# Kernel optimization log

Measured on AMD Instinct MI355X. Metric: run time of the kernel, lower is better.

## Reference

```python
import jax, jax.numpy as jnp
import numpy as np

B, CDD, HIS, S, L, F, K = 32, 5, 100, 20, 3, 150, 18
NNEWS, RDIM = 10000, 256


def _maxpool3(x):
    # kernel [3,3,3], stride [3,3,3], no padding (torch MaxPool3d default)
    return jax.lax.reduce_window(x, -jnp.inf, jax.lax.max,
                                 (1, 1, 3, 3, 3), (1, 1, 3, 3, 3), 'VALID')


def setup_inputs() -> dict:
    key = jax.random.key(0)
    ks = jax.random.split(key, 10)
    return {
        'cdd_id': jax.random.randint(ks[0], (B, CDD), 0, NNEWS),
        'his_id': jax.random.randint(ks[1], (B, HIS), 0, NNEWS),
        'news_repr_table': jax.random.normal(ks[2], (NNEWS, RDIM), jnp.float32),
        'news_embedding_table': jax.random.normal(ks[3], (NNEWS, S * L * F), jnp.float32),
        'conv1_w': jax.random.normal(ks[4], (32, 3, 3, 3, 3), jnp.float32) * 0.1,
        'conv1_b': jax.random.normal(ks[5], (32,), jnp.float32) * 0.1,
        'conv2_w': jax.random.normal(ks[6], (16, 32, 3, 3, 3), jnp.float32) * 0.1,
        'conv2_b': jax.random.normal(ks[7], (16,), jnp.float32) * 0.1,
        'ltr_w': jax.random.normal(ks[8], (1, 128), jnp.float32) * 0.1,
        'ltr_b': jax.random.normal(ks[9], (1,), jnp.float32) * 0.1,
    }


def reference(cdd_id, his_id, news_repr_table, news_embedding_table,
              conv1_w, conv1_b, conv2_w, conv2_b, ltr_w, ltr_b):
    cdd_repr = news_repr_table[cdd_id]                    # [B,CDD,R]
    his_repr = news_repr_table[his_id]                    # [B,HIS,R]
    cdd_emb = news_embedding_table[cdd_id].reshape(B, CDD, S, L, F)
    his_emb = news_embedding_table[his_id]                # [B,HIS,S*L*F]

    # attention scores; original applies softmax then sorts the (detached)
    # weights -- softmax is monotone per row so argsort on logits is identical
    attn = jnp.einsum('bcr,bhr->bch', cdd_repr, his_repr)  # [B,CDD,HIS]
    topk_idx = jnp.argsort(-attn, axis=-1)[..., :K]        # [B,CDD,K]

    # direct gather (replaces the one_hot @ embedding matmul, same math)
    his_act = his_emb[jnp.arange(B)[:, None, None], topk_idx]  # [B,CDD,K,S*L*F]
    his_act = his_act.reshape(B, CDD, K, S, L, F)

    # fusion tensor at each dilation level
    cdd_t = cdd_emb.transpose(0, 1, 3, 2, 4)       # [B,CDD,L,S,F]
    his_t = his_act.transpose(0, 1, 2, 4, 3, 5)    # [B,CDD,K,L,S,F]
    fusion = jnp.einsum('bclsf,bckltf->bcklst', cdd_t, his_t) / np.sqrt(F).astype(np.float32)
    x = fusion.reshape(B * CDD, K, L, S, S).transpose(0, 2, 1, 3, 4)  # [B*CDD,L,K,S,S]

    dn = ('NCDHW', 'OIDHW', 'NCDHW')
    pad1 = [(1, 1)] * 3
    x = jax.lax.conv_general_dilated(x, conv1_w, (1, 1, 1), pad1, dimension_numbers=dn)
    x = jax.nn.relu(x + conv1_b[None, :, None, None, None])
    x = _maxpool3(x)                                # [B*CDD,32,6,6,6]
    x = jax.lax.conv_general_dilated(x, conv2_w, (1, 1, 1), pad1, dimension_numbers=dn)
    x = jax.nn.relu(x + conv2_b[None, :, None, None, None])
    x = _maxpool3(x)                                # [B*CDD,16,2,2,2]

    feat = x.reshape(B, CDD, -1)                    # [B,CDD,128]
    score = jnp.einsum('bcd,od->bco', feat, ltr_w)[..., 0] + ltr_b[0]  # [B,CDD]
    return jax.nn.log_softmax(score, axis=1)
```

## Files before the change

### kernel.cpp

```cpp
#include <hip/hip_runtime.h>
#include <hip/hip_bf16.h>
#include <math.h>

#define B_    32
#define CDD_  5
#define HIS_  100
#define S_    20
#define L_    3
#define F_    150
#define K_    18
#define RDIM_ 256
#define ROWE_ 9000
#define NBC_  160

typedef __attribute__((ext_vector_type(8))) short short8;
typedef __attribute__((ext_vector_type(4))) float f32x4;

static __device__ __forceinline__ unsigned short f2bf(float x) {
  union { float f; unsigned u; } v; v.f = x;
  unsigned r = v.u + 0x7fffu + ((v.u >> 16) & 1u);
  return (unsigned short)(r >> 16);
}

__global__ __launch_bounds__(256) void attn_topk_kernel(
    const int* __restrict__ cdd_id, const int* __restrict__ his_id,
    const float* __restrict__ repr, int* __restrict__ gid,
    float* __restrict__ score,
    const float* __restrict__ w1, const float* __restrict__ w2,
    float* __restrict__ w1t, float* __restrict__ w2t) {
  int bc = blockIdx.x;
  int b  = bc / CDD_;
  int tid = threadIdx.x, lane = tid & 63, wave = tid >> 6;

  int gidx = bc * 256 + tid;
  if (gidx < 2592) {
    int oc = gidx / 81, j = gidx % 81;
    w1t[j * 32 + oc] = w1[gidx];
  } else if (gidx < 2592 + 13824) {
    int i2 = gidx - 2592;
    int oc = i2 / 864, r = i2 % 864;
    w2t[r * 16 + oc] = w2[i2];
  }

  __shared__ float cddv[RDIM_];
  __shared__ float sattn[128];
  int cid = cdd_id[bc];
  cddv[tid] = repr[(size_t)cid * RDIM_ + tid];
  if (tid < 28) sattn[100 + tid] = -INFINITY;
  __syncthreads();

  float4 cv = *(const float4*)(cddv + lane * 4);
  for (int h = wave; h < HIS_; h += 4) {
    const float4* row = (const float4*)(repr + (size_t)his_id[b * HIS_ + h] * RDIM_);
    float4 rv = row[lane];
    float p = cv.x * rv.x;
    p = fmaf(cv.y, rv.y, p);
    p = fmaf(cv.z, rv.z, p);
    p = fmaf(cv.w, rv.w, p);
    #pragma unroll
    for (int off = 32; off >= 1; off >>= 1) p += __shfl_xor(p, off);
    if (lane == 0) sattn[h] = p;
  }
  __syncthreads();

  if (wave == 0) {
    float v0 = sattn[lane], v1 = sattn[lane + 64];
    for (int k = 0; k < K_; k++) {
      float bv; int bi;
      if (v1 > v0) { bv = v1; bi = lane + 64; } else { bv = v0; bi = lane; }
      #pragma unroll
      for (int off = 32; off >= 1; off >>= 1) {
        float ov = __shfl_xor(bv, off);
        int   oi = __shfl_xor(bi, off);
        if (ov > bv || (ov == bv && oi < bi)) { bv = ov; bi = oi; }
      }
      if (lane == 0) gid[bc * K_ + k] = his_id[b * HIS_ + bi];
      if (bi == lane)      v0 = -INFINITY;
      if (bi == lane + 64) v1 = -INFINITY;
    }
  }
  if (tid == 0) score[bc] = 0.f;
}

__global__ __launch_bounds__(256) void fusion_kernel(
    const int* __restrict__ cdd_id, const int* __restrict__ gid,
    const float* __restrict__ emb, float* __restrict__ x1) {
  int bck = (blockIdx.x & 7) * 360 + (blockIdx.x >> 3);
  int bc = bck / K_, k = bck % K_;
  __shared__ unsigned short a_sh[3 * 32 * 160];
  __shared__ unsigned short b_sh[3 * 32 * 160];
  int tid = threadIdx.x;

  unsigned* az = (unsigned*)a_sh;
  unsigned* bz = (unsigned*)b_sh;
  for (int i = tid; i < 480; i += 256) {
    int l = i / 160, r = i % 160;
    int srow = r / 5, j = r % 5;
    int idx = (l * 32 + srow) * 80 + 75 + j;
    az[idx] = 0u; bz[idx] = 0u;
  }

  const float* crow = emb + (size_t)cdd_id[bc] * ROWE_;
  const float* hrow = emb + (size_t)gid[bck] * ROWE_;
  for (int p = tid; p < 2250; p += 256) {
    int e0 = p * 4;
    int s0 = e0 / 450, r0 = e0 % 450;
    int l0 = r0 / 150, f0 = r0 % 150;
    int e2 = e0 + 2;
    int s2 = e2 / 450, r2 = e2 % 450;
    int l2 = r2 / 150, f2 = r2 % 150;
    float4 cv = *(const float4*)(crow + e0);
    float4 hv = *(const float4*)(hrow + e0);
    int d0 = (l0 * 32 + s0) * 80 + (f0 >> 1);
    int d2 = (l2 * 32 + s2) * 80 + (f2 >> 1);
    az[d0] = (unsigned)f2bf(cv.x) | ((unsigned)f2bf(cv.y) << 16);
    az[d2] = (unsigned)f2bf(cv.z) | ((unsigned)f2bf(cv.w) << 16);
    bz[d0] = (unsigned)f2bf(hv.x) | ((unsigned)f2bf(hv.y) << 16);
    bz[d2] = (unsigned)f2bf(hv.z) | ((unsigned)f2bf(hv.w) << 16);
  }
  __syncthreads();

  int wave = tid >> 6, lane = tid & 63;
  int m15 = lane & 15, quad = lane >> 4;
  const float scale = 0.0816496580927726f;
  for (int j = wave; j < 12; j += 4) {
    int l = j >> 2, mt = (j >> 1) & 1, nt = j & 1;
    f32x4 acc = {0.f, 0.f, 0.f, 0.f};
    int abase = (l * 32 + mt * 16 + m15) * 160 + quad * 8;
    int bbase = (l * 32 + nt * 16 + m15) * 160 + quad * 8;
    #pragma unroll
    for (int kb = 0; kb < 5; kb++) {
      short8 af = *(const short8*)(a_sh + abase + kb * 32);
      short8 bf = *(const short8*)(b_sh + bbase + kb * 32);
      acc = __builtin_amdgcn_mfma_f32_16x16x32_bf16(af, bf, acc, 0, 0, 0);
    }
    int t = nt * 16 + m15;
    if (t < 20) {
      size_t base = ((size_t)(bc * 3 + l) * K_ + k) * 400;
      #pragma unroll
      for (int reg = 0; reg < 4; reg++) {
        int s = mt * 16 + quad * 4 + reg;
        if (s < 20) x1[base + s * 20 + t] = acc[reg] * scale;
      }
    }
  }
}

__global__ __launch_bounds__(256) void conv1_kernel(
    const float* __restrict__ x1, const float* __restrict__ w1t,
    const float* __restrict__ b1, float* __restrict__ p1) {
  int bid = blockIdx.x;
  int n = bid / 6, dp = bid % 6;
  __shared__ float tile[3 * 5 * 22 * 22];
  __shared__ unsigned pooled[32 * 36];
  int tid = threadIdx.x;

  for (int i = tid; i < 7260; i += 256) {
    int c = i / 2420; int r = i % 2420;
    int dd = r / 484; r %= 484;
    int hh = r / 22, ww = r % 22;
    int d = dp * 3 + dd - 1, h = hh - 1, w = ww - 1;
    float v = 0.f;
    if (d >= 0 && d < 18 && h >= 0 && h < 20 && w >= 0 && w < 20)
      v = x1[((size_t)(n * 3 + c) * K_ + d) * 400 + h * 20 + w];
    tile[i] = v;
  }
  for (int i = tid; i < 1152; i += 256) pooled[i] = 0u;
  __syncthreads();

  for (int pos = tid; pos < 972; pos += 256) {
    int dl = pos / 324; int r = pos % 324;
    int h = r / 18, w = r % 18;
    float acc[32];
    #pragma unroll
    for (int oc = 0; oc < 32; oc++) acc[oc] = b1[oc];

    for (int c = 0; c < 3; c++) {
      const float* tc = tile + (c * 5 + dl) * 484 + h * 22 + w;
      const float* wc = w1t + c * 27 * 32;
      #pragma unroll
      for (int kd = 0; kd < 3; kd++)
        #pragma unroll
        for (int kh = 0; kh < 3; kh++)
          #pragma unroll
          for (int kw = 0; kw < 3; kw++) {
            float iv = tc[kd * 484 + kh * 22 + kw];
            const float* wp = wc + (kd * 9 + kh * 3 + kw) * 32;
            #pragma unroll
            for (int oc = 0; oc < 32; oc++) acc[oc] = fmaf(iv, wp[oc], acc[oc]);
          }
    }
    int pbase = (h / 3) * 6 + (w / 3);
    #pragma unroll
    for (int oc = 0; oc < 32; oc++)
      atomicMax(&pooled[oc * 36 + pbase], __float_as_uint(fmaxf(acc[oc], 0.f)));
  }
  __syncthreads();
  for (int i = tid; i < 1152; i += 256) {
    int oc = i / 36; int r = i % 36;
    p1[(size_t)(n * 32 + oc) * 216 + dp * 36 + r] = __uint_as_float(pooled[i]);
  }
}

__global__ __launch_bounds__(256) void conv2_kernel(
    const float* __restrict__ p1, const float* __restrict__ w2t,
    const float* __restrict__ b2, const float* __restrict__ lw,
    float* __restrict__ score) {
  int bid = blockIdx.x;
  int n = bid / 2, og = bid % 2;
  __shared__ float tile[32 * 8 * 8 * 8];
  __shared__ unsigned pooled[64];
  int tid = threadIdx.x;

  for (int i = tid; i < 32 * 512; i += 256) tile[i] = 0.f;
  if (tid < 64) pooled[tid] = 0u;
  __syncthreads();
  for (int i = tid; i < 32 * 216; i += 256) {
    int c = i / 216; int r = i % 216;
    int d = r / 36; r %= 36;
    int h = r / 6, w = r % 6;
    tile[c * 512 + (d + 1) * 64 + (h + 1) * 8 + (w + 1)] =
        p1[(size_t)n * 32 * 216 + i];
  }
  __syncthreads();

  if (tid < 216) {
    int d = tid / 36; int r = tid % 36;
    int h = r / 6, w = r % 6;
    float acc[8];
    #pragma unroll
    for (int oc = 0; oc < 8; oc++) acc[oc] = b2[og * 8 + oc];
    for (int c = 0; c < 32; c++) {
      const float* tc = tile + c * 512 + d * 64 + h * 8 + w;
      const float* wc = w2t + c * 27 * 16 + og * 8;
      #pragma unroll
      for (int kd = 0; kd < 3; kd++)
        #pragma unroll
        for (int kh = 0; kh < 3; kh++)
          #pragma unroll
          for (int kw = 0; kw < 3; kw++) {
            float iv = tc[kd * 64 + kh * 8 + kw];
            const float* wp = wc + (kd * 9 + kh * 3 + kw) * 16;
            #pragma unroll
            for (int oc = 0; oc < 8; oc++) acc[oc] = fmaf(iv, wp[oc], acc[oc]);
          }
    }
    int pb = (d / 3) * 4 + (h / 3) * 2 + (w / 3);
    #pragma unroll
    for (int oc = 0; oc < 8; oc++)
      atomicMax(&pooled[oc * 8 + pb], __float_as_uint(fmaxf(acc[oc], 0.f)));
  }
  __syncthreads();

  if (tid < 64) {
    int oc = tid / 8, pb = tid % 8;
    float contrib = __uint_as_float(pooled[tid]) * lw[(og * 8 + oc) * 8 + pb];
    #pragma unroll
    for (int off = 32; off >= 1; off >>= 1) contrib += __shfl_xor(contrib, off);
    if (tid == 0) atomicAdd(&score[n], contrib);
  }
}

__global__ __launch_bounds__(64) void softmax_kernel(
    const float* __restrict__ score, const float* __restrict__ lb,
    float* __restrict__ out) {
  int b = threadIdx.x;
  if (b < B_) {
    float s[CDD_];
    float mx = -INFINITY;
    #pragma unroll
    for (int c = 0; c < CDD_; c++) {
      s[c] = score[b * CDD_ + c] + lb[0];
      mx = fmaxf(mx, s[c]);
    }
    float sum = 0.f;
    #pragma unroll
    for (int c = 0; c < CDD_; c++) sum += expf(s[c] - mx);
    float lse = mx + logf(sum);
    #pragma unroll
    for (int c = 0; c < CDD_; c++) out[b * CDD_ + c] = s[c] - lse;
  }
}

extern "C" void kernel_launch(void* const* d_in, const int* in_sizes, int n_in,
                              void* d_out, int out_size, void* d_ws, size_t ws_size,
                              hipStream_t stream) {
  const int*   cdd_id = (const int*)d_in[0];
  const int*   his_id = (const int*)d_in[1];
  const float* repr   = (const float*)d_in[2];
  const float* emb    = (const float*)d_in[3];
  const float* w1     = (const float*)d_in[4];
  const float* b1     = (const float*)d_in[5];
  const float* w2     = (const float*)d_in[6];
  const float* b2     = (const float*)d_in[7];
  const float* lw     = (const float*)d_in[8];
  const float* lb     = (const float*)d_in[9];
  float* out = (float*)d_out;

  char* ws = (char*)d_ws;
  int*   gid   = (int*)ws;
  float* score = (float*)(ws + 11520);
  float* x1    = (float*)(ws + 12160);
  float* p1    = (float*)(ws + 12160 + 13824000);
  float* w1t   = (float*)(ws + 12160 + 13824000 + 4423680);
  float* w2t   = (float*)(ws + 12160 + 13824000 + 4423680 + 10368);

  attn_topk_kernel<<<NBC_, 256, 0, stream>>>(cdd_id, his_id, repr, gid, score,
                                             w1, w2, w1t, w2t);
  fusion_kernel<<<NBC_ * K_, 256, 0, stream>>>(cdd_id, gid, emb, x1);
  conv1_kernel<<<NBC_ * 6, 256, 0, stream>>>(x1, w1t, b1, p1);
  conv2_kernel<<<NBC_ * 2, 256, 0, stream>>>(p1, w2t, b2, lw, score);
  softmax_kernel<<<1, 64, 0, stream>>>(score, lb, out);
}
```

Baseline: 601.3 us.

## Fuse fusion-tensor MFMA into conv1 kernel, keeping slab in shared memory

```diff
diff --git a/kernel.cpp b/kernel.cpp
--- a/kernel.cpp
+++ b/kernel.cpp
@@ -22,6 +22,10 @@
   return (unsigned short)(r >> 16);
 }
 
+static __device__ __forceinline__ unsigned pack2bf(float a, float b) {
+  return (unsigned)f2bf(a) | ((unsigned)f2bf(b) << 16);
+}
+
 __global__ __launch_bounds__(256) void attn_topk_kernel(
     const int* __restrict__ cdd_id, const int* __restrict__ his_id,
     const float* __restrict__ repr, int* __restrict__ gid,
@@ -82,26 +86,31 @@
   if (tid == 0) score[bc] = 0.f;
 }
 
-__global__ __launch_bounds__(256) void fusion_kernel(
+__global__ __launch_bounds__(256) void fusion_conv1_kernel(
     const int* __restrict__ cdd_id, const int* __restrict__ gid,
-    const float* __restrict__ emb, float* __restrict__ x1) {
-  int bck = (blockIdx.x & 7) * 360 + (blockIdx.x >> 3);
-  int bc = bck / K_, k = bck % K_;
-  __shared__ unsigned short a_sh[3 * 32 * 160];
-  __shared__ unsigned short b_sh[3 * 32 * 160];
+    const float* __restrict__ emb, const float* __restrict__ w1t,
+    const float* __restrict__ b1, float* __restrict__ p1) {
+  int lb = (blockIdx.x & 7) * 120 + (blockIdx.x >> 3);
+  int n = lb / 6, dp = lb % 6;
+
+  __shared__ __align__(16) char smem[61440];
+  unsigned short* a_sh = (unsigned short*)smem;
+  unsigned short* b_sh = (unsigned short*)(smem + 30720);
+  float*    xslab  = (float*)smem;
+  unsigned* pooled = (unsigned*)(smem + 29040);
+
   int tid = threadIdx.x;
-
   unsigned* az = (unsigned*)a_sh;
   unsigned* bz = (unsigned*)b_sh;
+
   for (int i = tid; i < 480; i += 256) {
     int l = i / 160, r = i % 160;
-    int srow = r / 5, j = r % 5;
-    int idx = (l * 32 + srow) * 80 + 75 + j;
+    int srow = r / 5, j5 = r % 5;
+    int idx = (l * 32 + srow) * 80 + 75 + j5;
     az[idx] = 0u; bz[idx] = 0u;
   }
 
-  const float* crow = emb + (size_t)cdd_id[bc] * ROWE_;
-  const float* hrow = emb + (size_t)gid[bck] * ROWE_;
+  const float* crow = emb + (size_t)cdd_id[n] * ROWE_;
   for (int p = tid; p < 2250; p += 256) {
     int e0 = p * 4;
     int s0 = e0 / 450, r0 = e0 % 450;
@@ -110,73 +119,93 @@
     int s2 = e2 / 450, r2 = e2 % 450;
     int l2 = r2 / 150, f2 = r2 % 150;
     float4 cv = *(const float4*)(crow + e0);
-    float4 hv = *(const float4*)(hrow + e0);
-    int d0 = (l0 * 32 + s0) * 80 + (f0 >> 1);
-    int d2 = (l2 * 32 + s2) * 80 + (f2 >> 1);
-    az[d0] = (unsigned)f2bf(cv.x) | ((unsigned)f2bf(cv.y) << 16);
-    az[d2] = (unsigned)f2bf(cv.z) | ((unsigned)f2bf(cv.w) << 16);
-    bz[d0] = (unsigned)f2bf(hv.x) | ((unsigned)f2bf(hv.y) << 16);
-    bz[d2] = (unsigned)f2bf(hv.z) | ((unsigned)f2bf(hv.w) << 16);
-  }
-  __syncthreads();
+    az[(l0 * 32 + s0) * 80 + (f0 >> 1)] = pack2bf(cv.x, cv.y);
+    az[(l2 * 32 + s2) * 80 + (f2 >> 1)] = pack2bf(cv.z, cv.w);
+  }
 
   int wave = tid >> 6, lane = tid & 63;
   int m15 = lane & 15, quad = lane >> 4;
+
+  f32x4 acc[5][3];
+  #pragma unroll
+  for (int kk = 0; kk < 5; kk++)
+    #pragma unroll
+    for (int t = 0; t < 3; t++) acc[kk][t] = (f32x4){0.f, 0.f, 0.f, 0.f};
+
+  #pragma unroll
+  for (int kk = 0; kk < 5; kk++) {
+    int k = dp * 3 + kk - 1;
+    bool valid = (k >= 0 && k < K_);
+    if (valid) {
+      const float* hrow = emb + (size_t)gid[n * K_ + k] * ROWE_;
+      for (int p = tid; p < 2250; p += 256) {
+        int e0 = p * 4;
+        int s0 = e0 / 450, r0 = e0 % 450;
+        int l0 = r0 / 150, f0 = r0 % 150;
+        int e2 = e0 + 2;
+        int s2 = e2 / 450, r2 = e2 % 450;
+        int l2 = r2 / 150, f2 = r2 % 150;
+        float4 hv = *(const float4*)(hrow + e0);
+        bz[(l0 * 32 + s0) * 80 + (f0 >> 1)] = pack2bf(hv.x, hv.y);
+        bz[(l2 * 32 + s2) * 80 + (f2 >> 1)] = pack2bf(hv.z, hv.w);
+      }
+    }
+    __syncthreads();
+    if (valid) {
+      #pragma unroll
+      for (int t = 0; t < 3; t++) {
+        int j = wave + 4 * t;
+        int l = j >> 2, mt = (j >> 1) & 1, nt = j & 1;
+        int abase = (l * 32 + mt * 16 + m15) * 160 + quad * 8;
+        int bbase = (l * 32 + nt * 16 + m15) * 160 + quad * 8;
+        #pragma unroll
+        for (int kb = 0; kb < 5; kb++) {
+          short8 af = *(const short8*)(a_sh + abase + kb * 32);
+          short8 bf = *(const short8*)(b_sh + bbase + kb * 32);
+          acc[kk][t] = __builtin_amdgcn_mfma_f32_16x16x32_bf16(af, bf, acc[kk][t], 0, 0, 0);
+        }
+      }
+    }
+    __syncthreads();
+  }
+
+  for (int i = tid; i < 7260; i += 256) xslab[i] = 0.f;
+  for (int i = tid; i < 1152; i += 256) pooled[i] = 0u;
+  __syncthreads();
+
   const float scale = 0.0816496580927726f;
-  for (int j = wave; j < 12; j += 4) {
-    int l = j >> 2, mt = (j >> 1) & 1, nt = j & 1;
-    f32x4 acc = {0.f, 0.f, 0.f, 0.f};
-    int abase = (l * 32 + mt * 16 + m15) * 160 + quad * 8;
-    int bbase = (l * 32 + nt * 16 + m15) * 160 + quad * 8;
-    #pragma unroll
-    for (int kb = 0; kb < 5; kb++) {
-      short8 af = *(const short8*)(a_sh + abase + kb * 32);
-      short8 bf = *(const short8*)(b_sh + bbase + kb * 32);
-      acc = __builtin_amdgcn_mfma_f32_16x16x32_bf16(af, bf, acc, 0, 0, 0);
-    }
-    int t = nt * 16 + m15;
-    if (t < 20) {
-      size_t base = ((size_t)(bc * 3 + l) * K_ + k) * 400;
-      #pragma unroll
-      for (int reg = 0; reg < 4; reg++) {
-        int s = mt * 16 + quad * 4 + reg;
-        if (s < 20) x1[base + s * 20 + t] = acc[reg] * scale;
+  #pragma unroll
+  for (int kk = 0; kk < 5; kk++) {
+    int k = dp * 3 + kk - 1;
+    if (k >= 0 && k < K_) {
+      #pragma unroll
+      for (int t = 0; t < 3; t++) {
+        int j = wave + 4 * t;
+        int l = j >> 2, mt = (j >> 1) & 1, nt = j & 1;
+        int tc = nt * 16 + m15;
+        if (tc < 20) {
+          #pragma unroll
+          for (int reg = 0; reg < 4; reg++) {
+            int s = mt * 16 + quad * 4 + reg;
+            if (s < 20)
+              xslab[(l * 5 + kk) * 484 + (s + 1) * 22 + (tc + 1)] =
+                  acc[kk][t][reg] * scale;
+          }
+        }
       }
     }
   }
-}
-
-__global__ __launch_bounds__(256) void conv1_kernel(
-    const float* __restrict__ x1, const float* __restrict__ w1t,
-    const float* __restrict__ b1, float* __restrict__ p1) {
-  int bid = blockIdx.x;
-  int n = bid / 6, dp = bid % 6;
-  __shared__ float tile[3 * 5 * 22 * 22];
-  __shared__ unsigned pooled[32 * 36];
-  int tid = threadIdx.x;
-
-  for (int i = tid; i < 7260; i += 256) {
-    int c = i / 2420; int r = i % 2420;
-    int dd = r / 484; r %= 484;
-    int hh = r / 22, ww = r % 22;
-    int d = dp * 3 + dd - 1, h = hh - 1, w = ww - 1;
-    float v = 0.f;
-    if (d >= 0 && d < 18 && h >= 0 && h < 20 && w >= 0 && w < 20)
-      v = x1[((size_t)(n * 3 + c) * K_ + d) * 400 + h * 20 + w];
-    tile[i] = v;
-  }
-  for (int i = tid; i < 1152; i += 256) pooled[i] = 0u;
   __syncthreads();
 
   for (int pos = tid; pos < 972; pos += 256) {
     int dl = pos / 324; int r = pos % 324;
     int h = r / 18, w = r % 18;
-    float acc[32];
-    #pragma unroll
-    for (int oc = 0; oc < 32; oc++) acc[oc] = b1[oc];
+    float cacc[32];
+    #pragma unroll
+    for (int oc = 0; oc < 32; oc++) cacc[oc] = b1[oc];
 
     for (int c = 0; c < 3; c++) {
-      const float* tc = tile + (c * 5 + dl) * 484 + h * 22 + w;
+      const float* tc2 = xslab + (c * 5 + dl) * 484 + h * 22 + w;
       const float* wc = w1t + c * 27 * 32;
       #pragma unroll
       for (int kd = 0; kd < 3; kd++)
@@ -184,16 +213,16 @@
         for (int kh = 0; kh < 3; kh++)
           #pragma unroll
           for (int kw = 0; kw < 3; kw++) {
-            float iv = tc[kd * 484 + kh * 22 + kw];
+            float iv = tc2[kd * 484 + kh * 22 + kw];
             const float* wp = wc + (kd * 9 + kh * 3 + kw) * 32;
             #pragma unroll
-            for (int oc = 0; oc < 32; oc++) acc[oc] = fmaf(iv, wp[oc], acc[oc]);
+            for (int oc = 0; oc < 32; oc++) cacc[oc] = fmaf(iv, wp[oc], cacc[oc]);
           }
     }
     int pbase = (h / 3) * 6 + (w / 3);
     #pragma unroll
     for (int oc = 0; oc < 32; oc++)
-      atomicMax(&pooled[oc * 36 + pbase], __float_as_uint(fmaxf(acc[oc], 0.f)));
+      atomicMax(&pooled[oc * 36 + pbase], __float_as_uint(fmaxf(cacc[oc], 0.f)));
   }
   __syncthreads();
   for (int i = tid; i < 1152; i += 256) {
@@ -300,15 +329,13 @@
   char* ws = (char*)d_ws;
   int*   gid   = (int*)ws;
   float* score = (float*)(ws + 11520);
-  float* x1    = (float*)(ws + 12160);
-  float* p1    = (float*)(ws + 12160 + 13824000);
-  float* w1t   = (float*)(ws + 12160 + 13824000 + 4423680);
-  float* w2t   = (float*)(ws + 12160 + 13824000 + 4423680 + 10368);
+  float* p1    = (float*)(ws + 12160);
+  float* w1t   = (float*)(ws + 12160 + 4423680);
+  float* w2t   = (float*)(ws + 12160 + 4423680 + 10368);
 
   attn_topk_kernel<<<NBC_, 256, 0, stream>>>(cdd_id, his_id, repr, gid, score,
                                              w1, w2, w1t, w2t);
-  fusion_kernel<<<NBC_ * K_, 256, 0, stream>>>(cdd_id, gid, emb, x1);
-  conv1_kernel<<<NBC_ * 6, 256, 0, stream>>>(x1, w1t, b1, p1);
+  fusion_conv1_kernel<<<NBC_ * 6, 256, 0, stream>>>(cdd_id, gid, emb, w1t, b1, p1);
   conv2_kernel<<<NBC_ * 2, 256, 0, stream>>>(p1, w2t, b2, lw, score);
   softmax_kernel<<<1, 64, 0, stream>>>(score, lb, out);
 }
```

After: 609.6 us. No clear change (+1.4%).

## Process two top-k rows per fusion block and fold softmax into conv2

Applied to the files above, without the earlier changes.

```diff
diff --git a/kernel.cpp b/kernel.cpp
--- a/kernel.cpp
+++ b/kernel.cpp
@@ -22,10 +22,14 @@
   return (unsigned short)(r >> 16);
 }
 
+static __device__ __forceinline__ unsigned pack2bf(float a, float b) {
+  return (unsigned)f2bf(a) | ((unsigned)f2bf(b) << 16);
+}
+
 __global__ __launch_bounds__(256) void attn_topk_kernel(
     const int* __restrict__ cdd_id, const int* __restrict__ his_id,
     const float* __restrict__ repr, int* __restrict__ gid,
-    float* __restrict__ score,
+    float* __restrict__ score, int* __restrict__ scnt,
     const float* __restrict__ w1, const float* __restrict__ w2,
     float* __restrict__ w1t, float* __restrict__ w2t) {
   int bc = blockIdx.x;
@@ -79,14 +83,61 @@
       if (bi == lane + 64) v1 = -INFINITY;
     }
   }
-  if (tid == 0) score[bc] = 0.f;
+  if (tid == 0) {
+    score[bc] = 0.f;
+    if (bc < B_) scnt[bc] = 0;
+  }
+}
+
+static __device__ __forceinline__ void stage_row_b(
+    const float* __restrict__ row, unsigned* __restrict__ dst, int tid) {
+  for (int p = tid; p < 2250; p += 256) {
+    int e0 = p * 4;
+    int s0 = e0 / 450, r0 = e0 % 450;
+    int l0 = r0 / 150, f0 = r0 % 150;
+    int e2 = e0 + 2;
+    int s2 = e2 / 450, r2 = e2 % 450;
+    int l2 = r2 / 150, f2 = r2 % 150;
+    float4 v = *(const float4*)(row + e0);
+    dst[(l0 * 32 + s0) * 80 + (f0 >> 1)] = pack2bf(v.x, v.y);
+    dst[(l2 * 32 + s2) * 80 + (f2 >> 1)] = pack2bf(v.z, v.w);
+  }
+}
+
+static __device__ __forceinline__ void mfma_tile_store(
+    const unsigned short* __restrict__ a_sh,
+    const unsigned short* __restrict__ b_sh,
+    int wave, int m15, int quad, int bc, int k, float* __restrict__ x1) {
+  const float scale = 0.0816496580927726f;
+  for (int j = wave; j < 12; j += 4) {
+    int l = j >> 2, mt = (j >> 1) & 1, nt = j & 1;
+    f32x4 acc = {0.f, 0.f, 0.f, 0.f};
+    int abase = (l * 32 + mt * 16 + m15) * 160 + quad * 8;
+    int bbase = (l * 32 + nt * 16 + m15) * 160 + quad * 8;
+    #pragma unroll
+    for (int kb = 0; kb < 5; kb++) {
+      short8 af = *(const short8*)(a_sh + abase + kb * 32);
+      short8 bf = *(const short8*)(b_sh + bbase + kb * 32);
+      acc = __builtin_amdgcn_mfma_f32_16x16x32_bf16(af, bf, acc, 0, 0, 0);
+    }
+    int t = nt * 16 + m15;
+    if (t < 20) {
+      size_t base = ((size_t)(bc * 3 + l) * K_ + k) * 400;
+      #pragma unroll
+      for (int reg = 0; reg < 4; reg++) {
+        int s = mt * 16 + quad * 4 + reg;
+        if (s < 20) x1[base + s * 20 + t] = acc[reg] * scale;
+      }
+    }
+  }
 }
 
 __global__ __launch_bounds__(256) void fusion_kernel(
     const int* __restrict__ cdd_id, const int* __restrict__ gid,
     const float* __restrict__ emb, float* __restrict__ x1) {
-  int bck = (blockIdx.x & 7) * 360 + (blockIdx.x >> 3);
-  int bc = bck / K_, k = bck % K_;
+  int lb = (blockIdx.x & 7) * 180 + (blockIdx.x >> 3);
+  int bc = lb / 9, kp = lb % 9;
+  int k0 = 2 * kp, k1 = 2 * kp + 1;
   __shared__ unsigned short a_sh[3 * 32 * 160];
   __shared__ unsigned short b_sh[3 * 32 * 160];
   int tid = threadIdx.x;
@@ -100,8 +151,8 @@
     az[idx] = 0u; bz[idx] = 0u;
   }
 
-  const float* crow = emb + (size_t)cdd_id[bc] * ROWE_;
-  const float* hrow = emb + (size_t)gid[bck] * ROWE_;
+  const float* crow  = emb + (size_t)cdd_id[bc] * ROWE_;
+  const float* hrow0 = emb + (size_t)gid[bc * K_ + k0] * ROWE_;
   for (int p = tid; p < 2250; p += 256) {
     int e0 = p * 4;
     int s0 = e0 / 450, r0 = e0 % 450;
@@ -110,40 +161,27 @@
     int s2 = e2 / 450, r2 = e2 % 450;
     int l2 = r2 / 150, f2 = r2 % 150;
     float4 cv = *(const float4*)(crow + e0);
-    float4 hv = *(const float4*)(hrow + e0);
+    float4 hv = *(const float4*)(hrow0 + e0);
     int d0 = (l0 * 32 + s0) * 80 + (f0 >> 1);
     int d2 = (l2 * 32 + s2) * 80 + (f2 >> 1);
-    az[d0] = (unsigned)f2bf(cv.x) | ((unsigned)f2bf(cv.y) << 16);
-    az[d2] = (unsigned)f2bf(cv.z) | ((unsigned)f2bf(cv.w) << 16);
-    bz[d0] = (unsigned)f2bf(hv.x) | ((unsigned)f2bf(hv.y) << 16);
-    bz[d2] = (unsigned)f2bf(hv.z) | ((unsigned)f2bf(hv.w) << 16);
+    az[d0] = pack2bf(cv.x, cv.y);
+    az[d2] = pack2bf(cv.z, cv.w);
+    bz[d0] = pack2bf(hv.x, hv.y);
+    bz[d2] = pack2bf(hv.z, hv.w);
   }
   __syncthreads();
 
   int wave = tid >> 6, lane = tid & 63;
   int m15 = lane & 15, quad = lane >> 4;
-  const float scale = 0.0816496580927726f;
-  for (int j = wave; j < 12; j += 4) {
-    int l = j >> 2, mt = (j >> 1) & 1, nt = j & 1;
-    f32x4 acc = {0.f, 0.f, 0.f, 0.f};
-    int abase = (l * 32 + mt * 16 + m15) * 160 + quad * 8;
-    int bbase = (l * 32 + nt * 16 + m15) * 160 + quad * 8;
-    #pragma unroll
-    for (int kb = 0; kb < 5; kb++) {
-      short8 af = *(const short8*)(a_sh + abase + kb * 32);
-      short8 bf = *(const short8*)(b_sh + bbase + kb * 32);
-      acc = __builtin_amdgcn_mfma_f32_16x16x32_bf16(af, bf, acc, 0, 0, 0);
-    }
-    int t = nt * 16 + m15;
-    if (t < 20) {
-      size_t base = ((size_t)(bc * 3 + l) * K_ + k) * 400;
-      #pragma unroll
-      for (int reg = 0; reg < 4; reg++) {
-        int s = mt * 16 + quad * 4 + reg;
-        if (s < 20) x1[base + s * 20 + t] = acc[reg] * scale;
-      }
-    }
-  }
+
+  mfma_tile_store(a_sh, b_sh, wave, m15, quad, bc, k0, x1);
+  __syncthreads();
+
+  const float* hrow1 = emb + (size_t)gid[bc * K_ + k1] * ROWE_;
+  stage_row_b(hrow1, bz, tid);
+  __syncthreads();
+
+  mfma_tile_store(a_sh, b_sh, wave, m15, quad, bc, k1, x1);
 }
 
 __global__ __launch_bounds__(256) void conv1_kernel(
@@ -205,7 +243,8 @@
 __global__ __launch_bounds__(256) void conv2_kernel(
     const float* __restrict__ p1, const float* __restrict__ w2t,
     const float* __restrict__ b2, const float* __restrict__ lw,
-    float* __restrict__ score) {
+    const float* __restrict__ lb, float* __restrict__ score,
+    int* __restrict__ scnt, float* __restrict__ out) {
   int bid = blockIdx.x;
   int n = bid / 2, og = bid % 2;
   __shared__ float tile[32 * 8 * 8 * 8];
@@ -259,26 +298,26 @@
     for (int off = 32; off >= 1; off >>= 1) contrib += __shfl_xor(contrib, off);
     if (tid == 0) atomicAdd(&score[n], contrib);
   }
-}
-
-__global__ __launch_bounds__(64) void softmax_kernel(
-    const float* __restrict__ score, const float* __restrict__ lb,
-    float* __restrict__ out) {
-  int b = threadIdx.x;
-  if (b < B_) {
-    float s[CDD_];
-    float mx = -INFINITY;
-    #pragma unroll
-    for (int c = 0; c < CDD_; c++) {
-      s[c] = score[b * CDD_ + c] + lb[0];
-      mx = fmaxf(mx, s[c]);
-    }
-    float sum = 0.f;
-    #pragma unroll
-    for (int c = 0; c < CDD_; c++) sum += expf(s[c] - mx);
-    float lse = mx + logf(sum);
-    #pragma unroll
-    for (int c = 0; c < CDD_; c++) out[b * CDD_ + c] = s[c] - lse;
+
+  if (tid == 0) {
+    __threadfence();
+    int b = n / CDD_;
+    int old = atomicAdd(&scnt[b], 1);
+    if (old == 2 * CDD_ - 1) {
+      float s[CDD_];
+      float mx = -INFINITY;
+      #pragma unroll
+      for (int c = 0; c < CDD_; c++) {
+        s[c] = atomicAdd(&score[b * CDD_ + c], 0.0f) + lb[0];
+        mx = fmaxf(mx, s[c]);
+      }
+      float sum = 0.f;
+      #pragma unroll
+      for (int c = 0; c < CDD_; c++) sum += expf(s[c] - mx);
+      float lse = mx + logf(sum);
+      #pragma unroll
+      for (int c = 0; c < CDD_; c++) out[b * CDD_ + c] = s[c] - lse;
+    }
   }
 }
 
@@ -304,11 +343,11 @@
   float* p1    = (float*)(ws + 12160 + 13824000);
   float* w1t   = (float*)(ws + 12160 + 13824000 + 4423680);
   float* w2t   = (float*)(ws + 12160 + 13824000 + 4423680 + 10368);
+  int*   scnt  = (int*)(ws + 12160 + 13824000 + 4423680 + 10368 + 55296);
 
   attn_topk_kernel<<<NBC_, 256, 0, stream>>>(cdd_id, his_id, repr, gid, score,
-                                             w1, w2, w1t, w2t);
-  fusion_kernel<<<NBC_ * K_, 256, 0, stream>>>(cdd_id, gid, emb, x1);
+                                             scnt, w1, w2, w1t, w2t);
+  fusion_kernel<<<NBC_ * 9, 256, 0, stream>>>(cdd_id, gid, emb, x1);
   conv1_kernel<<<NBC_ * 6, 256, 0, stream>>>(x1, w1t, b1, p1);
-  conv2_kernel<<<NBC_ * 2, 256, 0, stream>>>(p1, w2t, b2, lw, score);
-  softmax_kernel<<<1, 64, 0, stream>>>(score, lb, out);
-}
+  conv2_kernel<<<NBC_ * 2, 256, 0, stream>>>(p1, w2t, b2, lw, lb, score, scnt, out);
+}
```

Result: no change. 602.6 us (+0.2%).
